# Kernel tuning notes

Hardware: AMD Instinct MI355X
Metric: run time of the kernel (lower is better)

Reference implementation:

```python
import jax, jax.numpy as jnp
import numpy as np

N, E, G = 50000, 400000, 64          # nodes, edges, graphs in batch
IN_DIM, OUT_DIM = 64, 128
N_ETYPES, N_STEPS = 4, 8


def setup_inputs() -> dict:
    key = jax.random.key(0)
    ks = jax.random.split(key, 13)
    s = 1.0 / np.sqrt(OUT_DIM)
    u = lambda k, shp: jax.random.uniform(k, shp, jnp.float32, -s, s)
    return {
        "node_features": jax.random.normal(ks[0], (N, IN_DIM), jnp.float32),
        "src": jax.random.randint(ks[1], (E,), 0, N),
        "dst": jax.random.randint(ks[2], (E,), 0, N),
        "etype": jax.random.randint(ks[3], (E,), 0, N_ETYPES),
        "graph_ids": jax.random.randint(ks[4], (N,), 0, G),
        "Ws": u(ks[5], (N_ETYPES, OUT_DIM, OUT_DIM)),   # per-edge-type linear
        "bs": u(ks[6], (N_ETYPES, OUT_DIM)),
        "W_ih": u(ks[7], (3 * OUT_DIM, OUT_DIM)),        # GRUCell (r,z,n order)
        "W_hh": u(ks[8], (3 * OUT_DIM, OUT_DIM)),
        "b_ih": u(ks[9], (3 * OUT_DIM,)),
        "b_hh": u(ks[10], (3 * OUT_DIM,)),
        "W_cls": u(ks[11], (1, OUT_DIM + IN_DIM)),
        "b_cls": u(ks[12], (1,)),
    }


def _gru_cell(x, h, W_ih, W_hh, b_ih, b_hh):
    gi = x @ W_ih.T + b_ih
    gh = h @ W_hh.T + b_hh
    ir, iz, i_n = jnp.split(gi, 3, axis=-1)
    hr, hz, h_n = jnp.split(gh, 3, axis=-1)
    r = jax.nn.sigmoid(ir + hr)
    z = jax.nn.sigmoid(iz + hz)
    n = jnp.tanh(i_n + r * h_n)
    return (1.0 - z) * n + z * h


def reference(node_features, src, dst, etype, graph_ids,
              Ws, bs, W_ih, W_hh, b_ih, b_hh, W_cls, b_cls):
    # pad input features to OUT_DIM (GGNN.forward zero_pad)
    h = jnp.concatenate(
        [node_features, jnp.zeros((N, OUT_DIM - IN_DIM), node_features.dtype)], -1)

    def step(h, _):
        # per-edge-type linear transform of all node states: (T, N, D)
        Wh = jnp.einsum('nd,tkd->tnk', h, Ws) + bs[:, None, :]
        msg = Wh[etype, src]                                  # (E, D) gather
        a = jax.ops.segment_sum(msg, dst, num_segments=N)     # scatter-add
        return _gru_cell(a, h, W_ih, W_hh, b_ih, b_hh), None

    h, _ = jax.lax.scan(step, h, None, length=N_STEPS)

    hcat = jnp.concatenate([h, node_features], -1)            # (N, OUT+IN)
    feats = jax.ops.segment_sum(hcat, graph_ids, num_segments=G)  # sum readout
    return jax.nn.sigmoid(feats @ W_cls.T + b_cls)            # (G, 1)
```

## Files before the change

kernel.cpp:

```cpp
#include <hip/hip_runtime.h>
#include <hip/hip_bf16.h>
#include <math.h>


#define NN 50000
#define NE 400000
#define NG 64
#define IND 64
#define OD 128
#define LDO 896
#define RC 8

typedef _Float16 f16x8 __attribute__((ext_vector_type(8)));
typedef _Float16 f16x4 __attribute__((ext_vector_type(4)));
typedef _Float16 f16x2 __attribute__((ext_vector_type(2)));
typedef float f32x4 __attribute__((ext_vector_type(4)));

__device__ inline unsigned short f2h(float x) {
    _Float16 hv = (_Float16)x;
    unsigned short u;
    __builtin_memcpy(&u, &hv, 2);
    return u;
}

__global__ void k_cvt(const float* __restrict__ s, unsigned short* __restrict__ d, int n) {
    int i = blockIdx.x * 256 + threadIdx.x;
    if (i < n) d[i] = f2h(s[i]);
}

__global__ void k_init_h(const float* __restrict__ nf, float* __restrict__ h,
                         unsigned short* __restrict__ hb) {
    int i = blockIdx.x * 256 + threadIdx.x;
    if (i >= NN * OD) return;
    int n = i >> 7, d = i & 127;
    float v = (d < IND) ? nf[n * IND + d] : 0.f;
    h[i] = v;
    hb[i] = f2h(v);
}

__global__ void k_count(const int* __restrict__ dst, int* __restrict__ deg) {
    int e = blockIdx.x * 256 + threadIdx.x;
    if (e < NE) atomicAdd(&deg[dst[e]], 1);
}

__global__ void k_scan1(const int* __restrict__ deg, int* __restrict__ rowp,
                        int* __restrict__ bsum) {
    __shared__ int buf[1024];
    int tid = threadIdx.x;
    int i = blockIdx.x * 1024 + tid;
    int v = (i < NN) ? deg[i] : 0;
    buf[tid] = v;
    __syncthreads();
    for (int off = 1; off < 1024; off <<= 1) {
        int t = (tid >= off) ? buf[tid - off] : 0;
        __syncthreads();
        buf[tid] += t;
        __syncthreads();
    }
    if (i < NN) rowp[i + 1] = buf[tid];
    if (tid == 1023) bsum[blockIdx.x] = buf[tid];
}

__global__ void k_scan2(int* __restrict__ bsum, int nb) {
    __shared__ int buf[64];
    int tid = threadIdx.x;
    int v = (tid < nb) ? bsum[tid] : 0;
    buf[tid] = v;
    __syncthreads();
    for (int off = 1; off < 64; off <<= 1) {
        int t = (tid >= off) ? buf[tid - off] : 0;
        __syncthreads();
        buf[tid] += t;
        __syncthreads();
    }
    if (tid < nb) bsum[tid] = buf[tid] - v;
}

__global__ void k_scan3(const int* __restrict__ deg, const int* __restrict__ bsum,
                        int* __restrict__ rowp, int* __restrict__ cursor) {
    int i = blockIdx.x * 256 + threadIdx.x;
    if (i >= NN) return;
    int incl = rowp[i + 1] + bsum[i >> 10];
    rowp[i + 1] = incl;
    cursor[i] = incl - deg[i];
    if (i == 0) rowp[0] = 0;
}

__global__ void k_fill(const int* __restrict__ src, const int* __restrict__ dst,
                       const int* __restrict__ et, int* __restrict__ cursor,
                       int* __restrict__ ebase) {
    int e = blockIdx.x * 256 + threadIdx.x;
    if (e < NE) {
        int pos = atomicAdd(&cursor[dst[e]], 1);
        ebase[pos] = src[e] * LDO + et[e] * 128;
    }
}

__global__ void k_gcount(const int* __restrict__ gid, int* __restrict__ gdeg) {
    __shared__ int c[NG];
    int tid = threadIdx.x;
    if (tid < NG) c[tid] = 0;
    __syncthreads();
    int n = blockIdx.x * 1024 + tid;
    if (n < NN) atomicAdd(&c[gid[n]], 1);
    __syncthreads();
    if (tid < NG && c[tid] > 0) atomicAdd(&gdeg[tid], c[tid]);
}

__global__ void k_gscan(const int* __restrict__ gdeg, int* __restrict__ growp,
                        int* __restrict__ gcur) {
    __shared__ int buf[NG];
    int tid = threadIdx.x;
    int v = gdeg[tid];
    buf[tid] = v;
    __syncthreads();
    for (int off = 1; off < NG; off <<= 1) {
        int t = (tid >= off) ? buf[tid - off] : 0;
        __syncthreads();
        buf[tid] += t;
        __syncthreads();
    }
    growp[tid + 1] = buf[tid];
    gcur[tid] = buf[tid] - v;
    if (tid == 0) growp[0] = 0;
}

__global__ void k_gfill(const int* __restrict__ gid, int* __restrict__ gcur,
                        int* __restrict__ nlist) {
    __shared__ int lcnt[NG];
    __shared__ int lbase[NG];
    int tid = threadIdx.x;
    if (tid < NG) lcnt[tid] = 0;
    __syncthreads();
    int n = blockIdx.x * 1024 + tid;
    int g = -1, rank = 0;
    if (n < NN) { g = gid[n]; rank = atomicAdd(&lcnt[g], 1); }
    __syncthreads();
    if (tid < NG && lcnt[tid] > 0) lbase[tid] = atomicAdd(&gcur[tid], lcnt[tid]);
    __syncthreads();
    if (n < NN) nlist[lbase[g] + rank] = n;
}

__global__ __launch_bounds__(256) void k_gemm_mfma(
    const unsigned short* __restrict__ Ab, int M,
    const unsigned short* __restrict__ W0, const float* __restrict__ b0, int ngrp0,
    const unsigned short* __restrict__ W1, const float* __restrict__ b1,
    unsigned short* __restrict__ C) {
    __shared__ unsigned short As[128 * 136];
    __shared__ unsigned short Bs[128 * 136];

    const int g = blockIdx.y;
    const unsigned short* W;
    const float* bias;
    if (g < ngrp0) { W = W0 + (size_t)g * 16384; bias = b0 + g * 128; }
    else           { W = W1 + (size_t)(g - ngrp0) * 16384; bias = b1 + (g - ngrp0) * 128; }
    const int colbase = g * 128;
    const int m0 = blockIdx.x * 128;
    const int tid = threadIdx.x;

    const uint4* A4 = (const uint4*)Ab;
    const uint4* W4 = (const uint4*)W;

#pragma unroll
    for (int i = tid; i < 2048; i += 256) {
        int row = i >> 4, qq = i & 15;
        int n = m0 + row;
        uint4 va = (n < M) ? A4[(size_t)n * 16 + qq] : make_uint4(0u, 0u, 0u, 0u);
        *(uint4*)&As[row * 136 + qq * 8] = va;
        *(uint4*)&Bs[row * 136 + qq * 8] = W4[(size_t)row * 16 + qq];
    }
    __syncthreads();

    const int lane = tid & 63;
    const int w = tid >> 6;
    const int lr = lane & 15;
    const int q = lane >> 4;

    float bv[8];
#pragma unroll
    for (int nt = 0; nt < 8; ++nt) bv[nt] = bias[nt * 16 + lr];

    f32x4 acc[2][8];
#pragma unroll
    for (int mt = 0; mt < 2; ++mt)
#pragma unroll
        for (int nt = 0; nt < 8; ++nt) acc[mt][nt] = (f32x4){0.f, 0.f, 0.f, 0.f};

#pragma unroll
    for (int ks = 0; ks < 4; ++ks) {
        f16x8 af[2];
#pragma unroll
        for (int mt = 0; mt < 2; ++mt)
            af[mt] = *(const f16x8*)&As[(w * 32 + mt * 16 + lr) * 136 + ks * 32 + q * 8];
        f16x8 bfr[8];
#pragma unroll
        for (int nt = 0; nt < 8; ++nt)
            bfr[nt] = *(const f16x8*)&Bs[(nt * 16 + lr) * 136 + ks * 32 + q * 8];
#pragma unroll
        for (int mt = 0; mt < 2; ++mt)
#pragma unroll
            for (int nt = 0; nt < 8; ++nt)
                acc[mt][nt] = __builtin_amdgcn_mfma_f32_16x16x32_f16(
                    af[mt], bfr[nt], acc[mt][nt], 0, 0, 0);
    }

#pragma unroll
    for (int mt = 0; mt < 2; ++mt) {
        int rowbase = m0 + w * 32 + mt * 16 + q * 4;
#pragma unroll
        for (int r = 0; r < 4; ++r) {
            int n = rowbase + r;
            if (n < M) {
                unsigned short* crow = C + (size_t)n * LDO + colbase;
#pragma unroll
                for (int nt = 0; nt < 8; ++nt)
                    crow[nt * 16 + lr] = f2h(acc[mt][nt][r] + bv[nt]);
            }
        }
    }
}

__global__ void k_aggregate(const unsigned short* __restrict__ O,
                            const int* __restrict__ rowp, const int* __restrict__ ebase,
                            unsigned short* __restrict__ ab) {
    int wv = (blockIdx.x * 256 + threadIdx.x) >> 6;
    int lane = threadIdx.x & 63;
    int n = wv * 2 + (lane >> 5);
    if (n >= NN) return;
    int d4 = (lane & 31) * 4;
    int beg = rowp[n], end = rowp[n + 1];
    float a0 = 0.f, a1 = 0.f, a2 = 0.f, a3 = 0.f;
    for (int i = beg; i < end; ++i) {
        int b = ebase[i];
        f16x4 v = *(const f16x4*)&O[b + d4];
        a0 += (float)v[0]; a1 += (float)v[1]; a2 += (float)v[2]; a3 += (float)v[3];
    }
    f16x4 r;
    r[0] = (_Float16)a0; r[1] = (_Float16)a1; r[2] = (_Float16)a2; r[3] = (_Float16)a3;
    *(f16x4*)&ab[n * OD + d4] = r;
}

__global__ void k_gru(const unsigned short* __restrict__ O, float* __restrict__ h,
                      unsigned short* __restrict__ hb) {
    int i = blockIdx.x * 256 + threadIdx.x;
    if (i >= NN * 64) return;
    int n = i >> 6, p = (i & 63) * 2;
    const unsigned short* r = O + (size_t)n * LDO;
    f16x2 ir = *(const f16x2*)&r[p];
    f16x2 iz = *(const f16x2*)&r[128 + p];
    f16x2 in_ = *(const f16x2*)&r[256 + p];
    f16x2 hr = *(const f16x2*)&r[512 + p];
    f16x2 hz = *(const f16x2*)&r[640 + p];
    f16x2 hn = *(const f16x2*)&r[768 + p];
    float2 hv = *(const float2*)&h[(size_t)n * OD + p];
    float2 nh;
    {
        float rg = 1.f / (1.f + __expf(-((float)ir[0] + (float)hr[0])));
        float zg = 1.f / (1.f + __expf(-((float)iz[0] + (float)hz[0])));
        float ng = tanhf((float)in_[0] + rg * (float)hn[0]);
        nh.x = (1.f - zg) * ng + zg * hv.x;
        rg = 1.f / (1.f + __expf(-((float)ir[1] + (float)hr[1])));
        zg = 1.f / (1.f + __expf(-((float)iz[1] + (float)hz[1])));
        ng = tanhf((float)in_[1] + rg * (float)hn[1]);
        nh.y = (1.f - zg) * ng + zg * hv.y;
    }
    *(float2*)&h[(size_t)n * OD + p] = nh;
    f16x2 hb2; hb2[0] = (_Float16)nh.x; hb2[1] = (_Float16)nh.y;
    *(f16x2*)&hb[(size_t)n * OD + p] = hb2;
}

__global__ void k_readout(const float* __restrict__ h, const float* __restrict__ nf,
                          const int* __restrict__ nlist, const int* __restrict__ growp,
                          float* __restrict__ partial) {
    int g = blockIdx.x >> 3, c = blockIdx.x & (RC - 1);
    int d = threadIdx.x;
    int s = growp[g], e = growp[g + 1], len = e - s;
    int i0 = s + (int)((long long)len * c / RC);
    int i1 = s + (int)((long long)len * (c + 1) / RC);
    float acc = 0.f;
    for (int i = i0; i < i1; ++i) {
        int n = nlist[i];
        acc += (d < OD) ? h[(size_t)n * OD + d] : nf[(size_t)n * IND + (d - OD)];
    }
    partial[(size_t)blockIdx.x * 192 + d] = acc;
}

__global__ void k_reduce(const float* __restrict__ partial, float* __restrict__ feats) {
    int i = blockIdx.x * 256 + threadIdx.x;
    if (i >= NG * 192) return;
    int g = i / 192, d = i % 192;
    float s = 0.f;
    for (int c = 0; c < RC; ++c) s += partial[(size_t)(g * RC + c) * 192 + d];
    feats[i] = s;
}

__global__ void k_final(const float* __restrict__ feats, const float* __restrict__ W_cls,
                        const float* __restrict__ b_cls, float* __restrict__ out) {
    int g = threadIdx.x;
    if (g >= NG) return;
    float acc = b_cls[0];
    for (int d = 0; d < 192; ++d) acc += feats[g * 192 + d] * W_cls[d];
    out[g] = 1.f / (1.f + __expf(-acc));
}

extern "C" void kernel_launch(void* const* d_in, const int* in_sizes, int n_in,
                              void* d_out, int out_size, void* d_ws, size_t ws_size,
                              hipStream_t stream) {
    const float* nf    = (const float*)d_in[0];
    const int*   src   = (const int*)d_in[1];
    const int*   dst   = (const int*)d_in[2];
    const int*   et    = (const int*)d_in[3];
    const int*   gid   = (const int*)d_in[4];
    const float* Ws    = (const float*)d_in[5];
    const float* bs    = (const float*)d_in[6];
    const float* W_ih  = (const float*)d_in[7];
    const float* W_hh  = (const float*)d_in[8];
    const float* b_ih  = (const float*)d_in[9];
    const float* b_hh  = (const float*)d_in[10];
    const float* W_cls = (const float*)d_in[11];
    const float* b_cls = (const float*)d_in[12];
    float* out = (float*)d_out;

    char* ws = (char*)d_ws;
    size_t off = 0;
    auto alloc = [&](size_t bytes) -> void* {
        off = (off + 255) & ~(size_t)255;
        void* p = ws + off;
        off += bytes;
        return p;
    };
    float*          h    = (float*)alloc((size_t)NN * OD * 4);
    unsigned short* O    = (unsigned short*)alloc((size_t)NN * LDO * 2);
    unsigned short* hb   = (unsigned short*)alloc((size_t)NN * OD * 2);
    unsigned short* ab   = (unsigned short*)alloc((size_t)NN * OD * 2);
    int*   deg    = (int*)alloc((size_t)NN * 4);
    int*   rowp   = (int*)alloc((size_t)(NN + 1) * 4);
    int*   cursor = (int*)alloc((size_t)NN * 4);
    int*   ebase  = (int*)alloc((size_t)NE * 4);
    int*   bsum   = (int*)alloc(64 * 4);
    int*   gdeg   = (int*)alloc(NG * 4);
    int*   growp  = (int*)alloc((NG + 1) * 4);
    int*   gcur   = (int*)alloc(NG * 4);
    int*   nlist  = (int*)alloc((size_t)NN * 4);
    float* feats  = (float*)alloc((size_t)NG * 192 * 4);
    unsigned short* wsb  = (unsigned short*)alloc((size_t)4 * 16384 * 2);
    unsigned short* wihb = (unsigned short*)alloc((size_t)3 * 16384 * 2);
    unsigned short* whhb = (unsigned short*)alloc((size_t)3 * 16384 * 2);
    (void)ws_size; (void)in_sizes; (void)n_in; (void)out_size;

    float* partial = (float*)O;

    hipMemsetAsync(deg, 0, (size_t)NN * 4, stream);
    hipMemsetAsync(gdeg, 0, NG * 4, stream);

    k_cvt<<<(4 * 16384 + 255) / 256, 256, 0, stream>>>(Ws, wsb, 4 * 16384);
    k_cvt<<<(3 * 16384 + 255) / 256, 256, 0, stream>>>(W_ih, wihb, 3 * 16384);
    k_cvt<<<(3 * 16384 + 255) / 256, 256, 0, stream>>>(W_hh, whhb, 3 * 16384);

    k_init_h<<<(NN * OD + 255) / 256, 256, 0, stream>>>(nf, h, hb);
    k_count<<<(NE + 255) / 256, 256, 0, stream>>>(dst, deg);
    const int nb = (NN + 1023) / 1024;
    k_scan1<<<nb, 1024, 0, stream>>>(deg, rowp, bsum);
    k_scan2<<<1, 64, 0, stream>>>(bsum, nb);
    k_scan3<<<(NN + 255) / 256, 256, 0, stream>>>(deg, bsum, rowp, cursor);
    k_fill<<<(NE + 255) / 256, 256, 0, stream>>>(src, dst, et, cursor, ebase);

    k_gcount<<<nb, 1024, 0, stream>>>(gid, gdeg);
    k_gscan<<<1, NG, 0, stream>>>(gdeg, growp, gcur);
    k_gfill<<<nb, 1024, 0, stream>>>(gid, gcur, nlist);

    const int mt = (NN + 127) / 128;
    const int aggblk = (NN * 32 + 255) / 256;
    for (int s = 0; s < 8; ++s) {
        k_gemm_mfma<<<dim3(mt, 7), 256, 0, stream>>>(hb, NN, wsb, bs, 4, whhb, b_hh, O);
        k_aggregate<<<aggblk, 256, 0, stream>>>(O, rowp, ebase, ab);
        k_gemm_mfma<<<dim3(mt, 3), 256, 0, stream>>>(ab, NN, wihb, b_ih, 3, wihb, b_ih, O);
        k_gru<<<(NN * 64 + 255) / 256, 256, 0, stream>>>(O, h, hb);
    }

    k_readout<<<NG * RC, 192, 0, stream>>>(h, nf, nlist, growp, partial);
    k_reduce<<<(NG * 192 + 255) / 256, 256, 0, stream>>>(partial, feats);
    k_final<<<1, 64, 0, stream>>>(feats, W_cls, b_cls, out);
}
```

Before: 1.100 ms.

## Aggregate raw states per edge type before transform, fusing gather with per-type GEMM

Uses linearity to sum source hidden states per (dst, etype) bucket first and then apply each edge-type weight matrix, with bias scaled by per-type degree. This removes the wide 4x128 per-node message tensor the old code wrote and then gathered. The CSR is rebuilt keyed by dst*4+etype, and the input-side and hidden-side gate GEMMs are merged into one launch. The cost is a per-thread 64-float register accumulator in the gather phase, which may spill or lower occupancy, and gathers that read hb directly from global memory with uneven per-row edge counts.

```diff
diff --git a/kernel.cpp b/kernel.cpp
--- a/kernel.cpp
+++ b/kernel.cpp
@@ -8,7 +8,8 @@
 #define NG 64
 #define IND 64
 #define OD 128
-#define LDO 896
+#define NN4 (NN * 4)
+#define LDO 768
 #define RC 8
 
 typedef _Float16 f16x8 __attribute__((ext_vector_type(8)));
@@ -38,17 +39,18 @@
     hb[i] = f2h(v);
 }
 
-__global__ void k_count(const int* __restrict__ dst, int* __restrict__ deg) {
+__global__ void k_count(const int* __restrict__ dst, const int* __restrict__ et,
+                        int* __restrict__ deg4) {
     int e = blockIdx.x * 256 + threadIdx.x;
-    if (e < NE) atomicAdd(&deg[dst[e]], 1);
+    if (e < NE) atomicAdd(&deg4[dst[e] * 4 + et[e]], 1);
 }
 
 __global__ void k_scan1(const int* __restrict__ deg, int* __restrict__ rowp,
-                        int* __restrict__ bsum) {
+                        int* __restrict__ bsum, int n) {
     __shared__ int buf[1024];
     int tid = threadIdx.x;
     int i = blockIdx.x * 1024 + tid;
-    int v = (i < NN) ? deg[i] : 0;
+    int v = (i < n) ? deg[i] : 0;
     buf[tid] = v;
     __syncthreads();
     for (int off = 1; off < 1024; off <<= 1) {
@@ -57,17 +59,17 @@
         buf[tid] += t;
         __syncthreads();
     }
-    if (i < NN) rowp[i + 1] = buf[tid];
+    if (i < n) rowp[i + 1] = buf[tid];
     if (tid == 1023) bsum[blockIdx.x] = buf[tid];
 }
 
 __global__ void k_scan2(int* __restrict__ bsum, int nb) {
-    __shared__ int buf[64];
+    __shared__ int buf[256];
     int tid = threadIdx.x;
     int v = (tid < nb) ? bsum[tid] : 0;
     buf[tid] = v;
     __syncthreads();
-    for (int off = 1; off < 64; off <<= 1) {
+    for (int off = 1; off < 256; off <<= 1) {
         int t = (tid >= off) ? buf[tid - off] : 0;
         __syncthreads();
         buf[tid] += t;
@@ -77,9 +79,9 @@
 }
 
 __global__ void k_scan3(const int* __restrict__ deg, const int* __restrict__ bsum,
-                        int* __restrict__ rowp, int* __restrict__ cursor) {
+                        int* __restrict__ rowp, int* __restrict__ cursor, int n) {
     int i = blockIdx.x * 256 + threadIdx.x;
-    if (i >= NN) return;
+    if (i >= n) return;
     int incl = rowp[i + 1] + bsum[i >> 10];
     rowp[i + 1] = incl;
     cursor[i] = incl - deg[i];
@@ -88,11 +90,11 @@
 
 __global__ void k_fill(const int* __restrict__ src, const int* __restrict__ dst,
                        const int* __restrict__ et, int* __restrict__ cursor,
-                       int* __restrict__ ebase) {
+                       int* __restrict__ esrc) {
     int e = blockIdx.x * 256 + threadIdx.x;
     if (e < NE) {
-        int pos = atomicAdd(&cursor[dst[e]], 1);
-        ebase[pos] = src[e] * LDO + et[e] * 128;
+        int pos = atomicAdd(&cursor[dst[e] * 4 + et[e]], 1);
+        esrc[pos] = src[e];
     }
 }
 
@@ -141,41 +143,139 @@
     if (n < NN) nlist[lbase[g] + rank] = n;
 }
 
-__global__ __launch_bounds__(256) void k_gemm_mfma(
-    const unsigned short* __restrict__ Ab, int M,
-    const unsigned short* __restrict__ W0, const float* __restrict__ b0, int ngrp0,
-    const unsigned short* __restrict__ W1, const float* __restrict__ b1,
-    unsigned short* __restrict__ C) {
-    __shared__ unsigned short As[128 * 136];
-    __shared__ unsigned short Bs[128 * 136];
-
-    const int g = blockIdx.y;
-    const unsigned short* W;
-    const float* bias;
-    if (g < ngrp0) { W = W0 + (size_t)g * 16384; bias = b0 + g * 128; }
-    else           { W = W1 + (size_t)(g - ngrp0) * 16384; bias = b1 + (g - ngrp0) * 128; }
-    const int colbase = g * 128;
+__global__ __launch_bounds__(256) void k_agg_gemm(
+    const unsigned short* __restrict__ hb,
+    const int* __restrict__ rowp4, const int* __restrict__ esrc,
+    const int* __restrict__ deg4,
+    const unsigned short* __restrict__ Wsb,
+    const float* __restrict__ bs,
+    unsigned short* __restrict__ ab) {
+    __shared__ unsigned short Ss[128 * 136];
+    __shared__ float Bsb[512];
+
+    const int tid = threadIdx.x;
     const int m0 = blockIdx.x * 128;
-    const int tid = threadIdx.x;
-
-    const uint4* A4 = (const uint4*)Ab;
-    const uint4* W4 = (const uint4*)W;
-
-#pragma unroll
-    for (int i = tid; i < 2048; i += 256) {
-        int row = i >> 4, qq = i & 15;
-        int n = m0 + row;
-        uint4 va = (n < M) ? A4[(size_t)n * 16 + qq] : make_uint4(0u, 0u, 0u, 0u);
-        *(uint4*)&As[row * 136 + qq * 8] = va;
-        *(uint4*)&Bs[row * 136 + qq * 8] = W4[(size_t)row * 16 + qq];
-    }
-    __syncthreads();
+
+    Bsb[tid] = bs[tid];
+    Bsb[tid + 256] = bs[tid + 256];
+
+    const int r = tid >> 1;
+    const int hsel = tid & 1;
+    const int n = m0 + r;
 
     const int lane = tid & 63;
     const int w = tid >> 6;
     const int lr = lane & 15;
     const int q = lane >> 4;
 
+    f32x4 acc[2][8];
+#pragma unroll
+    for (int mt = 0; mt < 2; ++mt)
+#pragma unroll
+        for (int nt = 0; nt < 8; ++nt) acc[mt][nt] = (f32x4){0.f, 0.f, 0.f, 0.f};
+
+    for (int t = 0; t < 4; ++t) {
+        float sacc[64];
+#pragma unroll
+        for (int j = 0; j < 64; ++j) sacc[j] = 0.f;
+        if (n < NN) {
+            int beg = rowp4[n * 4 + t], end = rowp4[n * 4 + t + 1];
+            for (int i = beg; i < end; ++i) {
+                const f16x8* row8 = (const f16x8*)&hb[(size_t)esrc[i] * 128 + hsel * 64];
+#pragma unroll
+                for (int jj = 0; jj < 8; ++jj) {
+                    f16x8 v = row8[jj];
+#pragma unroll
+                    for (int k = 0; k < 8; ++k) sacc[jj * 8 + k] += (float)v[k];
+                }
+            }
+        }
+        __syncthreads();
+#pragma unroll
+        for (int jj = 0; jj < 8; ++jj) {
+            f16x8 hv;
+#pragma unroll
+            for (int k = 0; k < 8; ++k) hv[k] = (_Float16)sacc[jj * 8 + k];
+            *(f16x8*)&Ss[r * 136 + hsel * 64 + jj * 8] = hv;
+        }
+        __syncthreads();
+
+        const unsigned short* Wt = Wsb + t * 16384;
+#pragma unroll
+        for (int ks = 0; ks < 4; ++ks) {
+            f16x8 af[2];
+#pragma unroll
+            for (int mt = 0; mt < 2; ++mt)
+                af[mt] = *(const f16x8*)&Ss[(w * 32 + mt * 16 + lr) * 136 + ks * 32 + q * 8];
+#pragma unroll
+            for (int nt = 0; nt < 8; ++nt) {
+                f16x8 bf = *(const f16x8*)&Wt[(nt * 16 + lr) * 128 + ks * 32 + q * 8];
+#pragma unroll
+                for (int mt = 0; mt < 2; ++mt)
+                    acc[mt][nt] = __builtin_amdgcn_mfma_f32_16x16x32_f16(
+                        af[mt], bf, acc[mt][nt], 0, 0, 0);
+            }
+        }
+    }
+
+#pragma unroll
+    for (int mt = 0; mt < 2; ++mt) {
+        int rowbase = m0 + w * 32 + mt * 16 + q * 4;
+#pragma unroll
+        for (int rr = 0; rr < 4; ++rr) {
+            int n2 = rowbase + rr;
+            if (n2 < NN) {
+                int4 c = *(const int4*)&deg4[n2 * 4];
+                unsigned short* arow = ab + (size_t)n2 * 128;
+#pragma unroll
+                for (int nt = 0; nt < 8; ++nt) {
+                    int col = nt * 16 + lr;
+                    float v = acc[mt][nt][rr]
+                            + c.x * Bsb[col] + c.y * Bsb[128 + col]
+                            + c.z * Bsb[256 + col] + c.w * Bsb[384 + col];
+                    arow[col] = f2h(v);
+                }
+            }
+        }
+    }
+}
+
+__global__ __launch_bounds__(256) void k_gates_gemm(
+    const unsigned short* __restrict__ Aab, const unsigned short* __restrict__ Ahb,
+    int M,
+    const unsigned short* __restrict__ Wih, const unsigned short* __restrict__ Whh,
+    const float* __restrict__ bih, const float* __restrict__ bhh,
+    unsigned short* __restrict__ C) {
+    __shared__ unsigned short As[128 * 136];
+    __shared__ unsigned short Bs[128 * 136];
+
+    const int g = blockIdx.y;
+    const unsigned short* Ab = (g < 3) ? Aab : Ahb;
+    const unsigned short* W  = (g < 3) ? (Wih + (size_t)g * 16384)
+                                       : (Whh + (size_t)(g - 3) * 16384);
+    const float* bias = (g < 3) ? (bih + g * 128) : (bhh + (g - 3) * 128);
+    const int colbase = g * 128;
+    const int m0 = blockIdx.x * 128;
+    const int tid = threadIdx.x;
+
+    const uint4* A4 = (const uint4*)Ab;
+    const uint4* W4 = (const uint4*)W;
+
+#pragma unroll
+    for (int i = tid; i < 2048; i += 256) {
+        int row = i >> 4, qq = i & 15;
+        int nn = m0 + row;
+        uint4 va = (nn < M) ? A4[(size_t)nn * 16 + qq] : make_uint4(0u, 0u, 0u, 0u);
+        *(uint4*)&As[row * 136 + qq * 8] = va;
+        *(uint4*)&Bs[row * 136 + qq * 8] = W4[(size_t)row * 16 + qq];
+    }
+    __syncthreads();
+
+    const int lane = tid & 63;
+    const int w = tid >> 6;
+    const int lr = lane & 15;
+    const int q = lane >> 4;
+
     float bv[8];
 #pragma unroll
     for (int nt = 0; nt < 8; ++nt) bv[nt] = bias[nt * 16 + lr];
@@ -208,36 +308,16 @@
     for (int mt = 0; mt < 2; ++mt) {
         int rowbase = m0 + w * 32 + mt * 16 + q * 4;
 #pragma unroll
-        for (int r = 0; r < 4; ++r) {
-            int n = rowbase + r;
-            if (n < M) {
-                unsigned short* crow = C + (size_t)n * LDO + colbase;
+        for (int rr = 0; rr < 4; ++rr) {
+            int nn = rowbase + rr;
+            if (nn < M) {
+                unsigned short* crow = C + (size_t)nn * LDO + colbase;
 #pragma unroll
                 for (int nt = 0; nt < 8; ++nt)
-                    crow[nt * 16 + lr] = f2h(acc[mt][nt][r] + bv[nt]);
+                    crow[nt * 16 + lr] = f2h(acc[mt][nt][rr] + bv[nt]);
             }
         }
     }
-}
-
-__global__ void k_aggregate(const unsigned short* __restrict__ O,
-                            const int* __restrict__ rowp, const int* __restrict__ ebase,
-                            unsigned short* __restrict__ ab) {
-    int wv = (blockIdx.x * 256 + threadIdx.x) >> 6;
-    int lane = threadIdx.x & 63;
-    int n = wv * 2 + (lane >> 5);
-    if (n >= NN) return;
-    int d4 = (lane & 31) * 4;
-    int beg = rowp[n], end = rowp[n + 1];
-    float a0 = 0.f, a1 = 0.f, a2 = 0.f, a3 = 0.f;
-    for (int i = beg; i < end; ++i) {
-        int b = ebase[i];
-        f16x4 v = *(const f16x4*)&O[b + d4];
-        a0 += (float)v[0]; a1 += (float)v[1]; a2 += (float)v[2]; a3 += (float)v[3];
-    }
-    f16x4 r;
-    r[0] = (_Float16)a0; r[1] = (_Float16)a1; r[2] = (_Float16)a2; r[3] = (_Float16)a3;
-    *(f16x4*)&ab[n * OD + d4] = r;
 }
 
 __global__ void k_gru(const unsigned short* __restrict__ O, float* __restrict__ h,
@@ -249,9 +329,9 @@
     f16x2 ir = *(const f16x2*)&r[p];
     f16x2 iz = *(const f16x2*)&r[128 + p];
     f16x2 in_ = *(const f16x2*)&r[256 + p];
-    f16x2 hr = *(const f16x2*)&r[512 + p];
-    f16x2 hz = *(const f16x2*)&r[640 + p];
-    f16x2 hn = *(const f16x2*)&r[768 + p];
+    f16x2 hr = *(const f16x2*)&r[384 + p];
+    f16x2 hz = *(const f16x2*)&r[512 + p];
+    f16x2 hn = *(const f16x2*)&r[640 + p];
     float2 hv = *(const float2*)&h[(size_t)n * OD + p];
     float2 nh;
     {
@@ -333,16 +413,16 @@
     unsigned short* O    = (unsigned short*)alloc((size_t)NN * LDO * 2);
     unsigned short* hb   = (unsigned short*)alloc((size_t)NN * OD * 2);
     unsigned short* ab   = (unsigned short*)alloc((size_t)NN * OD * 2);
-    int*   deg    = (int*)alloc((size_t)NN * 4);
-    int*   rowp   = (int*)alloc((size_t)(NN + 1) * 4);
-    int*   cursor = (int*)alloc((size_t)NN * 4);
-    int*   ebase  = (int*)alloc((size_t)NE * 4);
-    int*   bsum   = (int*)alloc(64 * 4);
-    int*   gdeg   = (int*)alloc(NG * 4);
-    int*   growp  = (int*)alloc((NG + 1) * 4);
-    int*   gcur   = (int*)alloc(NG * 4);
-    int*   nlist  = (int*)alloc((size_t)NN * 4);
-    float* feats  = (float*)alloc((size_t)NG * 192 * 4);
+    int*   deg4    = (int*)alloc((size_t)NN4 * 4);
+    int*   rowp4   = (int*)alloc((size_t)(NN4 + 1) * 4);
+    int*   cursor4 = (int*)alloc((size_t)NN4 * 4);
+    int*   esrc    = (int*)alloc((size_t)NE * 4);
+    int*   bsum    = (int*)alloc(256 * 4);
+    int*   gdeg    = (int*)alloc(NG * 4);
+    int*   growp   = (int*)alloc((NG + 1) * 4);
+    int*   gcur    = (int*)alloc(NG * 4);
+    int*   nlist   = (int*)alloc((size_t)NN * 4);
+    float* feats   = (float*)alloc((size_t)NG * 192 * 4);
     unsigned short* wsb  = (unsigned short*)alloc((size_t)4 * 16384 * 2);
     unsigned short* wihb = (unsigned short*)alloc((size_t)3 * 16384 * 2);
     unsigned short* whhb = (unsigned short*)alloc((size_t)3 * 16384 * 2);
@@ -350,7 +430,7 @@
 
     float* partial = (float*)O;
 
-    hipMemsetAsync(deg, 0, (size_t)NN * 4, stream);
+    hipMemsetAsync(deg4, 0, (size_t)NN4 * 4, stream);
     hipMemsetAsync(gdeg, 0, NG * 4, stream);
 
     k_cvt<<<(4 * 16384 + 255) / 256, 256, 0, stream>>>(Ws, wsb, 4 * 16384);
@@ -358,23 +438,24 @@
     k_cvt<<<(3 * 16384 + 255) / 256, 256, 0, stream>>>(W_hh, whhb, 3 * 16384);
 
     k_init_h<<<(NN * OD + 255) / 256, 256, 0, stream>>>(nf, h, hb);
-    k_count<<<(NE + 255) / 256, 256, 0, stream>>>(dst, deg);
-    const int nb = (NN + 1023) / 1024;
-    k_scan1<<<nb, 1024, 0, stream>>>(deg, rowp, bsum);
-    k_scan2<<<1, 64, 0, stream>>>(bsum, nb);
-    k_scan3<<<(NN + 255) / 256, 256, 0, stream>>>(deg, bsum, rowp, cursor);
-    k_fill<<<(NE + 255) / 256, 256, 0, stream>>>(src, dst, et, cursor, ebase);
-
-    k_gcount<<<nb, 1024, 0, stream>>>(gid, gdeg);
+
+    k_count<<<(NE + 255) / 256, 256, 0, stream>>>(dst, et, deg4);
+    const int nb4 = (NN4 + 1023) / 1024;
+    k_scan1<<<nb4, 1024, 0, stream>>>(deg4, rowp4, bsum, NN4);
+    k_scan2<<<1, 256, 0, stream>>>(bsum, nb4);
+    k_scan3<<<(NN4 + 255) / 256, 256, 0, stream>>>(deg4, bsum, rowp4, cursor4, NN4);
+    k_fill<<<(NE + 255) / 256, 256, 0, stream>>>(src, dst, et, cursor4, esrc);
+
+    const int nbn = (NN + 1023) / 1024;
+    k_gcount<<<nbn, 1024, 0, stream>>>(gid, gdeg);
     k_gscan<<<1, NG, 0, stream>>>(gdeg, growp, gcur);
-    k_gfill<<<nb, 1024, 0, stream>>>(gid, gcur, nlist);
+    k_gfill<<<nbn, 1024, 0, stream>>>(gid, gcur, nlist);
 
     const int mt = (NN + 127) / 128;
-    const int aggblk = (NN * 32 + 255) / 256;
     for (int s = 0; s < 8; ++s) {
-        k_gemm_mfma<<<dim3(mt, 7), 256, 0, stream>>>(hb, NN, wsb, bs, 4, whhb, b_hh, O);
-        k_aggregate<<<aggblk, 256, 0, stream>>>(O, rowp, ebase, ab);
-        k_gemm_mfma<<<dim3(mt, 3), 256, 0, stream>>>(ab, NN, wihb, b_ih, 3, wihb, b_ih, O);
+        k_agg_gemm<<<mt, 256, 0, stream>>>(hb, rowp4, esrc, deg4, wsb, bs, ab);
+        k_gates_gemm<<<dim3(mt, 6), 256, 0, stream>>>(ab, hb, NN, wihb, whhb,
+                                                      b_ih, b_hh, O);
         k_gru<<<(NN * 64 + 255) / 256, 256, 0, stream>>>(O, h, hb);
     }
 
```

Measured after the change: 1.165 ms. 6.0% more time.
